# Kernel optimization log

Measured on AMD Instinct MI355X. Metric: run time of the kernel, lower is better.

## Reference

```python
import jax, jax.numpy as jnp
import numpy as np


def setup_inputs() -> dict:
    key = jax.random.key(0)
    ks = jax.random.split(key, 4)
    B, Tq, Tv, D = 8, 256, 512, 256  # decoder_dim = D = 256
    query = jax.random.normal(ks[0], (B, Tq, D), dtype=jnp.float32)
    value = jax.random.normal(ks[1], (B, Tv, D), dtype=jnp.float32)
    W1 = jax.random.normal(ks[2], (D, D), dtype=jnp.float32) * (1.0 / np.sqrt(D))
    b1 = jnp.zeros((D,), dtype=jnp.float32)
    W2 = jax.random.normal(ks[3], (D, D), dtype=jnp.float32) * (1.0 / np.sqrt(D))
    b2 = jnp.zeros((D,), dtype=jnp.float32)
    return {"query": query, "value": value, "W1": W1, "b1": b1, "W2": W2, "b2": b2}


def reference(query, value, W1, b1, W2, b2):
    # Dense projections: [B,Tq,D], [B,Tv,D]
    q = jnp.einsum('bqd,de->bqe', query, W1) + b1
    v = jnp.einsum('bvd,de->bve', value, W2) + b2
    # Additive (Bahdanau) score: broadcast tanh then reduce over feature dim
    # score: [B,Tq,Tv]  (intermediate [B,Tq,Tv,D] is the fusion target)
    score = jnp.tanh(q[:, :, None, :] + v[:, None, :, :]).sum(axis=-1)
    alignment = jax.nn.softmax(score, axis=-1)  # [B,Tq,Tv]
    context = jnp.einsum('bqv,bvd->bqd', alignment, value)  # [B,Tq,D]
    context = jnp.concatenate([context, query], axis=-1)  # [B,Tq,2D]
    alignment_t = jnp.transpose(alignment, (0, 2, 1))  # [B,Tv,Tq]
    return context, alignment_t
```

## Files before the change

kernel.cpp:

```cpp
#include <hip/hip_runtime.h>

#define B_  8
#define TQ  256
#define TV  512
#define DD  256
#define ALGS 520

__device__ __forceinline__ float fast_exp2(float x) {
#if __has_builtin(__builtin_amdgcn_exp2f)
  return __builtin_amdgcn_exp2f(x);
#else
  return __exp2f(x);
#endif
}
__device__ __forceinline__ float fast_rcp(float x) {
#if __has_builtin(__builtin_amdgcn_rcpf)
  return __builtin_amdgcn_rcpf(x);
#else
  return 1.0f / x;
#endif
}

__global__ __launch_bounds__(256) void proj_fused(
    const float* __restrict__ query, const float* __restrict__ value,
    const float* __restrict__ W1, const float* __restrict__ b1,
    const float* __restrict__ W2, const float* __restrict__ b2,
    float* __restrict__ qp, float* __restrict__ vp, float scale) {
  __shared__ float As[2][32][64];
  __shared__ float Bs[2][32][64];
  const int t  = threadIdx.x;
  const int rt = blockIdx.x;
  const int bn = blockIdx.y << 6;

  const float* A; const float* W; const float* bias; float* out; int row0;
  if (rt < 32) { row0 = rt << 6;        A = query; W = W1; bias = b1; out = qp; }
  else         { row0 = (rt - 32) << 6; A = value; W = W2; bias = b2; out = vp; }

  const int tx = t & 15, ty = t >> 4;
  const int aar = t >> 3, aac = (t & 7) << 2;
  const int bbr = t >> 4, bbc = (t & 15) << 2;

  float4 ra[2], rb[2];
#pragma unroll
  for (int it = 0; it < 2; ++it) {
    ra[it] = *(const float4*)(A + (size_t)(row0 + (it << 5) + aar) * DD + aac);
    rb[it] = *(const float4*)(W + (size_t)((it << 4) + bbr) * DD + bn + bbc);
  }
#pragma unroll
  for (int it = 0; it < 2; ++it) {
    const int m = (it << 5) + aar;
#pragma unroll
    for (int c = 0; c < 4; ++c) {
      const int k = aac + c;
      As[0][k][m ^ (((k >> 2) & 7) << 2)] = (&ra[it].x)[c];
    }
    *(float4*)&Bs[0][(it << 4) + bbr][bbc] = rb[it];
  }
  __syncthreads();

  float acc[4][4] = {{0.f,0.f,0.f,0.f},{0.f,0.f,0.f,0.f},
                     {0.f,0.f,0.f,0.f},{0.f,0.f,0.f,0.f}};
  int p = 0;

  for (int k0 = 0; k0 < 256; k0 += 32) {
    const bool more = (k0 + 32) < 256;
    if (more) {
#pragma unroll
      for (int it = 0; it < 2; ++it) {
        ra[it] = *(const float4*)(A + (size_t)(row0 + (it << 5) + aar) * DD + k0 + 32 + aac);
        rb[it] = *(const float4*)(W + (size_t)(k0 + 32 + (it << 4) + bbr) * DD + bn + bbc);
      }
    }
#pragma unroll
    for (int k = 0; k < 32; ++k) {
      float4 aq = *(const float4*)&As[p][k][(ty << 2) ^ (((k >> 2) & 7) << 2)];
      float4 bq = *(const float4*)&Bs[p][k][tx << 2];
      acc[0][0] = fmaf(aq.x, bq.x, acc[0][0]); acc[0][1] = fmaf(aq.x, bq.y, acc[0][1]);
      acc[0][2] = fmaf(aq.x, bq.z, acc[0][2]); acc[0][3] = fmaf(aq.x, bq.w, acc[0][3]);
      acc[1][0] = fmaf(aq.y, bq.x, acc[1][0]); acc[1][1] = fmaf(aq.y, bq.y, acc[1][1]);
      acc[1][2] = fmaf(aq.y, bq.z, acc[1][2]); acc[1][3] = fmaf(aq.y, bq.w, acc[1][3]);
      acc[2][0] = fmaf(aq.z, bq.x, acc[2][0]); acc[2][1] = fmaf(aq.z, bq.y, acc[2][1]);
      acc[2][2] = fmaf(aq.z, bq.z, acc[2][2]); acc[2][3] = fmaf(aq.z, bq.w, acc[2][3]);
      acc[3][0] = fmaf(aq.w, bq.x, acc[3][0]); acc[3][1] = fmaf(aq.w, bq.y, acc[3][1]);
      acc[3][2] = fmaf(aq.w, bq.z, acc[3][2]); acc[3][3] = fmaf(aq.w, bq.w, acc[3][3]);
    }
    if (more) {
      const int q = p ^ 1;
#pragma unroll
      for (int it = 0; it < 2; ++it) {
        const int m = (it << 5) + aar;
#pragma unroll
        for (int c = 0; c < 4; ++c) {
          const int k = aac + c;
          As[q][k][m ^ (((k >> 2) & 7) << 2)] = (&ra[it].x)[c];
        }
        *(float4*)&Bs[q][(it << 4) + bbr][bbc] = rb[it];
      }
      __syncthreads();
      p = q;
    }
  }

  float4 bvv = *(const float4*)&bias[bn + (tx << 2)];
#pragma unroll
  for (int r = 0; r < 4; ++r) {
    float4 o;
    o.x = fast_exp2(scale * (acc[r][0] + bvv.x));
    o.y = fast_exp2(scale * (acc[r][1] + bvv.y));
    o.z = fast_exp2(scale * (acc[r][2] + bvv.z));
    o.w = fast_exp2(scale * (acc[r][3] + bvv.w));
    *(float4*)(out + (size_t)(row0 + (ty << 2) + r) * DD + bn + (tx << 2)) = o;
  }
}

__global__ __launch_bounds__(512, 8) void attn_mono(
    const float* __restrict__ qp, const float* __restrict__ vp,
    const float* __restrict__ value, const float* __restrict__ query,
    float* __restrict__ out1, float* __restrict__ out2) {
  __shared__ float qs[4 * 256];
  __shared__ float alg[4 * ALGS];
  __shared__ float ctxp[8][4][128];

  const int t    = threadIdx.x;
  const int lane = t & 63;
  const int wv   = t >> 6;
  const int jj   = lane >> 2;
  const int dq   = lane & 3;
  const int bb   = blockIdx.x & 7;
  const int i0   = (blockIdx.x >> 3) << 2;

  const float* vpb = vp + (size_t)bb * TV * DD;
  const float* qb  = qp + (size_t)(bb * TQ + i0) * DD;

  {
    const int qi = t >> 7, qc = (t & 127) << 1;
    *(float2*)&qs[qi * 256 + qc] = *(const float2*)(qb + (size_t)qi * DD + qc);
  }
  __syncthreads();

  const int jb = (wv << 4) + jj;
  const float* vr0 = vpb + (size_t)jb * DD + (dq << 2);
  const float* vr1 = vr0 + 128 * DD;
  const float* vr2 = vr0 + 256 * DD;
  const float* vr3 = vr0 + 384 * DD;
  const float* qlane = qs + (dq << 2);

  float acc[4][4] = {{0.f,0.f,0.f,0.f},{0.f,0.f,0.f,0.f},
                     {0.f,0.f,0.f,0.f},{0.f,0.f,0.f,0.f}};

#pragma unroll 4
  for (int k = 0; k < 16; ++k) {
    const int doff = k << 4;
    float4 q0 = *(const float4*)(qlane + 0 * 256 + doff);
    float4 q1 = *(const float4*)(qlane + 1 * 256 + doff);
    float4 q2 = *(const float4*)(qlane + 2 * 256 + doff);
    float4 q3 = *(const float4*)(qlane + 3 * 256 + doff);
#pragma unroll
    for (int jg = 0; jg < 4; ++jg) {
      const float* vrp = (jg == 0) ? vr0 : (jg == 1) ? vr1 : (jg == 2) ? vr2 : vr3;
      float4 v4 = *(const float4*)(vrp + doff);
#pragma unroll
      for (int i = 0; i < 4; ++i) {
        const float4 q4 = (i == 0) ? q0 : (i == 1) ? q1 : (i == 2) ? q2 : q3;
        float a = q4.x * v4.x, b = q4.y * v4.y;
        float c = q4.z * v4.z, d = q4.w * v4.w;
        float sab = a + b,  scd = c + d;
        float Q1 = fmaf(a, b, sab + 1.f);
        float Q2 = fmaf(c, d, scd + 1.f);
        float N  = fmaf(scd + 2.f, Q1, (sab + 2.f) * Q2);
        acc[i][jg] = fmaf(N, fast_rcp(Q1 * Q2), acc[i][jg]);
      }
    }
  }

#pragma unroll
  for (int i = 0; i < 4; ++i)
#pragma unroll
    for (int jg = 0; jg < 4; ++jg) {
      acc[i][jg] += __shfl_xor(acc[i][jg], 1, 64);
      acc[i][jg] += __shfl_xor(acc[i][jg], 2, 64);
    }
#pragma unroll
  for (int jg = 0; jg < 4; ++jg) {
    float x = (dq == 0) ? acc[0][jg] : (dq == 1) ? acc[1][jg]
            : (dq == 2) ? acc[2][jg] : acc[3][jg];
    alg[dq * ALGS + (jg << 7) + jb] = x;
  }

  const int f4 = (t & 63) << 2;
  const int s  = t >> 6;
  const float* vb  = value + (size_t)bb * TV * DD;
  const float* vsp = vb + (size_t)(s << 6) * DD + f4;

  float4 pv0 = *(const float4*)(vsp + 0 * DD);
  float4 pv1 = *(const float4*)(vsp + 1 * DD);
  float4 pv2 = *(const float4*)(vsp + 2 * DD);
  float4 pv3 = *(const float4*)(vsp + 3 * DD);

  __syncthreads();

  if (wv < 4) {
    float sv[8];
#pragma unroll
    for (int c = 0; c < 8; ++c) sv[c] = alg[wv * ALGS + (c << 6) + lane];
    float mn = sv[0];
#pragma unroll
    for (int c = 1; c < 8; ++c) mn = fminf(mn, sv[c]);
#pragma unroll
    for (int m = 1; m < 64; m <<= 1) mn = fminf(mn, __shfl_xor(mn, m, 64));

    const float CC = 2.8853900817779268f;
    float p[8];
    float sum = 0.f;
#pragma unroll
    for (int c = 0; c < 8; ++c) { p[c] = fast_exp2(CC * (mn - sv[c])); sum += p[c]; }
#pragma unroll
    for (int m = 1; m < 64; m <<= 1) sum += __shfl_xor(sum, m, 64);
    const float inv = fast_rcp(sum);
#pragma unroll
    for (int c = 0; c < 8; ++c) alg[wv * ALGS + (c << 6) + lane] = p[c] * inv;
  }
  __syncthreads();

  {
    const int j = t;
    float4 av = make_float4(alg[j], alg[ALGS + j], alg[2 * ALGS + j], alg[3 * ALGS + j]);
    *(float4*)(out2 + (size_t)(bb * TV + j) * TQ + i0) = av;
  }

  float c4[4][4] = {{0.f,0.f,0.f,0.f},{0.f,0.f,0.f,0.f},
                    {0.f,0.f,0.f,0.f},{0.f,0.f,0.f,0.f}};
  const int jbase = s << 6;
  {
#pragma unroll
    for (int i = 0; i < 4; ++i) {
      float4 ai = *(const float4*)&alg[i * ALGS + jbase];
      c4[i][0] = fmaf(ai.x, pv0.x, c4[i][0]); c4[i][1] = fmaf(ai.x, pv0.y, c4[i][1]);
      c4[i][2] = fmaf(ai.x, pv0.z, c4[i][2]); c4[i][3] = fmaf(ai.x, pv0.w, c4[i][3]);
      c4[i][0] = fmaf(ai.y, pv1.x, c4[i][0]); c4[i][1] = fmaf(ai.y, pv1.y, c4[i][1]);
      c4[i][2] = fmaf(ai.y, pv1.z, c4[i][2]); c4[i][3] = fmaf(ai.y, pv1.w, c4[i][3]);
      c4[i][0] = fmaf(ai.z, pv2.x, c4[i][0]); c4[i][1] = fmaf(ai.z, pv2.y, c4[i][1]);
      c4[i][2] = fmaf(ai.z, pv2.z, c4[i][2]); c4[i][3] = fmaf(ai.z, pv2.w, c4[i][3]);
      c4[i][0] = fmaf(ai.w, pv3.x, c4[i][0]); c4[i][1] = fmaf(ai.w, pv3.y, c4[i][1]);
      c4[i][2] = fmaf(ai.w, pv3.z, c4[i][2]); c4[i][3] = fmaf(ai.w, pv3.w, c4[i][3]);
    }
  }
#pragma unroll 4
  for (int u = 4; u < 64; u += 4) {
    float4 v0 = *(const float4*)(vsp + (size_t)(u + 0) * DD);
    float4 v1 = *(const float4*)(vsp + (size_t)(u + 1) * DD);
    float4 v2 = *(const float4*)(vsp + (size_t)(u + 2) * DD);
    float4 v3 = *(const float4*)(vsp + (size_t)(u + 3) * DD);
#pragma unroll
    for (int i = 0; i < 4; ++i) {
      float4 ai = *(const float4*)&alg[i * ALGS + jbase + u];
      c4[i][0] = fmaf(ai.x, v0.x, c4[i][0]); c4[i][1] = fmaf(ai.x, v0.y, c4[i][1]);
      c4[i][2] = fmaf(ai.x, v0.z, c4[i][2]); c4[i][3] = fmaf(ai.x, v0.w, c4[i][3]);
      c4[i][0] = fmaf(ai.y, v1.x, c4[i][0]); c4[i][1] = fmaf(ai.y, v1.y, c4[i][1]);
      c4[i][2] = fmaf(ai.y, v1.z, c4[i][2]); c4[i][3] = fmaf(ai.y, v1.w, c4[i][3]);
      c4[i][0] = fmaf(ai.z, v2.x, c4[i][0]); c4[i][1] = fmaf(ai.z, v2.y, c4[i][1]);
      c4[i][2] = fmaf(ai.z, v2.z, c4[i][2]); c4[i][3] = fmaf(ai.z, v2.w, c4[i][3]);
      c4[i][0] = fmaf(ai.w, v3.x, c4[i][0]); c4[i][1] = fmaf(ai.w, v3.y, c4[i][1]);
      c4[i][2] = fmaf(ai.w, v3.z, c4[i][2]); c4[i][3] = fmaf(ai.w, v3.w, c4[i][3]);
    }
  }

  const float* qg = query + (size_t)(bb * TQ + i0) * DD;
  float* o = out1 + (size_t)(bb * TQ + i0) * (2 * DD);
#pragma unroll
  for (int h = 0; h < 2; ++h) {
    if ((f4 >> 7) == h) {
      const int fi = f4 & 127;
#pragma unroll
      for (int i = 0; i < 4; ++i)
        *(float4*)&ctxp[s][i][fi] = make_float4(c4[i][0], c4[i][1], c4[i][2], c4[i][3]);
    }
    __syncthreads();
    {
      const int ri = t >> 7;
      const int ff = t & 127;
      float sum = 0.f;
#pragma unroll
      for (int ss = 0; ss < 8; ++ss) sum += ctxp[ss][ri][ff];
      o[ri * 512 + (h << 7) + ff] = sum;
      o[ri * 512 + 256 + (h << 7) + ff] = qg[ri * DD + (h << 7) + ff];
    }
    if (h == 0) __syncthreads();
  }
}

extern "C" void kernel_launch(void* const* d_in, const int* in_sizes, int n_in,
                              void* d_out, int out_size, void* d_ws, size_t ws_size,
                              hipStream_t stream) {
  const float* query = (const float*)d_in[0];
  const float* value = (const float*)d_in[1];
  const float* W1    = (const float*)d_in[2];
  const float* b1    = (const float*)d_in[3];
  const float* W2    = (const float*)d_in[4];
  const float* b2    = (const float*)d_in[5];

  float* out1 = (float*)d_out;
  float* out2 = out1 + (size_t)B_ * TQ * 2 * DD;

  float* qp = (float*)d_ws;
  float* vp = qp + (size_t)B_ * TQ * DD;

  const float SC = 2.8853900817779268f;

  proj_fused<<<dim3(96, 4), 256, 0, stream>>>(query, value, W1, b1, W2, b2, qp, vp, SC);
  attn_mono<<<dim3(B_ * (TQ / 4)), 512, 0, stream>>>(qp, vp, value, query, out1, out2);
}
```

Measured before the change: 129.9 us.

## Double attention block to 1024 threads, splitting feature dimension across wave halves

The attention kernel now launches 1024 threads per block. The two halves of the block each compute the tanh score over half of the feature dimension and combine their partial scores in shared memory with an extra barrier. The context accumulation splits the value rows across 16 waves instead of 8. The goal is more parallelism per block, which shortens each thread's serial score loop. In exchange it adds a shared-memory add pass, another sync and a larger partial-context buffer, and at 1024 threads per block occupancy may be limited by registers.

```diff
diff --git a/kernel.cpp b/kernel.cpp
--- a/kernel.cpp
+++ b/kernel.cpp
@@ -113,17 +113,19 @@
   }
 }
 
-__global__ __launch_bounds__(512, 8) void attn_mono(
+__global__ __launch_bounds__(1024, 8) void attn_mono(
     const float* __restrict__ qp, const float* __restrict__ vp,
     const float* __restrict__ value, const float* __restrict__ query,
     float* __restrict__ out1, float* __restrict__ out2) {
   __shared__ float qs[4 * 256];
   __shared__ float alg[4 * ALGS];
-  __shared__ float ctxp[8][4][128];
+  __shared__ float ctxp[16][4][128];
 
   const int t    = threadIdx.x;
   const int lane = t & 63;
-  const int wv   = t >> 6;
+  const int w    = t >> 6;
+  const int wv   = w & 7;
+  const int dh   = w >> 3;
   const int jj   = lane >> 2;
   const int dq   = lane & 3;
   const int bb   = blockIdx.x & 7;
@@ -132,24 +134,22 @@
   const float* vpb = vp + (size_t)bb * TV * DD;
   const float* qb  = qp + (size_t)(bb * TQ + i0) * DD;
 
-  {
-    const int qi = t >> 7, qc = (t & 127) << 1;
-    *(float2*)&qs[qi * 256 + qc] = *(const float2*)(qb + (size_t)qi * DD + qc);
-  }
+  qs[t] = qb[(size_t)(t >> 8) * DD + (t & 255)];
   __syncthreads();
 
   const int jb = (wv << 4) + jj;
-  const float* vr0 = vpb + (size_t)jb * DD + (dq << 2);
+  const int d0 = dh << 7;
+  const float* vr0 = vpb + (size_t)jb * DD + d0 + (dq << 2);
   const float* vr1 = vr0 + 128 * DD;
   const float* vr2 = vr0 + 256 * DD;
   const float* vr3 = vr0 + 384 * DD;
-  const float* qlane = qs + (dq << 2);
+  const float* qlane = qs + d0 + (dq << 2);
 
   float acc[4][4] = {{0.f,0.f,0.f,0.f},{0.f,0.f,0.f,0.f},
                      {0.f,0.f,0.f,0.f},{0.f,0.f,0.f,0.f}};
 
 #pragma unroll 4
-  for (int k = 0; k < 16; ++k) {
+  for (int k = 0; k < 8; ++k) {
     const int doff = k << 4;
     float4 q0 = *(const float4*)(qlane + 0 * 256 + doff);
     float4 q1 = *(const float4*)(qlane + 1 * 256 + doff);
@@ -180,17 +180,22 @@
       acc[i][jg] += __shfl_xor(acc[i][jg], 1, 64);
       acc[i][jg] += __shfl_xor(acc[i][jg], 2, 64);
     }
-#pragma unroll
-  for (int jg = 0; jg < 4; ++jg) {
-    float x = (dq == 0) ? acc[0][jg] : (dq == 1) ? acc[1][jg]
-            : (dq == 2) ? acc[2][jg] : acc[3][jg];
-    alg[dq * ALGS + (jg << 7) + jb] = x;
+
+  float xh[4];
+#pragma unroll
+  for (int jg = 0; jg < 4; ++jg)
+    xh[jg] = (dq == 0) ? acc[0][jg] : (dq == 1) ? acc[1][jg]
+           : (dq == 2) ? acc[2][jg] : acc[3][jg];
+
+  if (dh == 0) {
+#pragma unroll
+    for (int jg = 0; jg < 4; ++jg) alg[dq * ALGS + (jg << 7) + jb] = xh[jg];
   }
 
   const int f4 = (t & 63) << 2;
   const int s  = t >> 6;
   const float* vb  = value + (size_t)bb * TV * DD;
-  const float* vsp = vb + (size_t)(s << 6) * DD + f4;
+  const float* vsp = vb + (size_t)(s << 5) * DD + f4;
 
   float4 pv0 = *(const float4*)(vsp + 0 * DD);
   float4 pv1 = *(const float4*)(vsp + 1 * DD);
@@ -198,11 +203,16 @@
   float4 pv3 = *(const float4*)(vsp + 3 * DD);
 
   __syncthreads();
-
-  if (wv < 4) {
+  if (dh == 1) {
+#pragma unroll
+    for (int jg = 0; jg < 4; ++jg) alg[dq * ALGS + (jg << 7) + jb] += xh[jg];
+  }
+  __syncthreads();
+
+  if (w < 4) {
     float sv[8];
 #pragma unroll
-    for (int c = 0; c < 8; ++c) sv[c] = alg[wv * ALGS + (c << 6) + lane];
+    for (int c = 0; c < 8; ++c) sv[c] = alg[w * ALGS + (c << 6) + lane];
     float mn = sv[0];
 #pragma unroll
     for (int c = 1; c < 8; ++c) mn = fminf(mn, sv[c]);
@@ -218,11 +228,11 @@
     for (int m = 1; m < 64; m <<= 1) sum += __shfl_xor(sum, m, 64);
     const float inv = fast_rcp(sum);
 #pragma unroll
-    for (int c = 0; c < 8; ++c) alg[wv * ALGS + (c << 6) + lane] = p[c] * inv;
-  }
-  __syncthreads();
-
-  {
+    for (int c = 0; c < 8; ++c) alg[w * ALGS + (c << 6) + lane] = p[c] * inv;
+  }
+  __syncthreads();
+
+  if (t < 512) {
     const int j = t;
     float4 av = make_float4(alg[j], alg[ALGS + j], alg[2 * ALGS + j], alg[3 * ALGS + j]);
     *(float4*)(out2 + (size_t)(bb * TV + j) * TQ + i0) = av;
@@ -230,7 +240,7 @@
 
   float c4[4][4] = {{0.f,0.f,0.f,0.f},{0.f,0.f,0.f,0.f},
                     {0.f,0.f,0.f,0.f},{0.f,0.f,0.f,0.f}};
-  const int jbase = s << 6;
+  const int jbase = s << 5;
   {
 #pragma unroll
     for (int i = 0; i < 4; ++i) {
@@ -245,8 +255,8 @@
       c4[i][2] = fmaf(ai.w, pv3.z, c4[i][2]); c4[i][3] = fmaf(ai.w, pv3.w, c4[i][3]);
     }
   }
-#pragma unroll 4
-  for (int u = 4; u < 64; u += 4) {
+#pragma unroll
+  for (int u = 4; u < 32; u += 4) {
     float4 v0 = *(const float4*)(vsp + (size_t)(u + 0) * DD);
     float4 v1 = *(const float4*)(vsp + (size_t)(u + 1) * DD);
     float4 v2 = *(const float4*)(vsp + (size_t)(u + 2) * DD);
@@ -276,12 +286,12 @@
         *(float4*)&ctxp[s][i][fi] = make_float4(c4[i][0], c4[i][1], c4[i][2], c4[i][3]);
     }
     __syncthreads();
-    {
+    if (t < 512) {
       const int ri = t >> 7;
       const int ff = t & 127;
       float sum = 0.f;
 #pragma unroll
-      for (int ss = 0; ss < 8; ++ss) sum += ctxp[ss][ri][ff];
+      for (int ss = 0; ss < 16; ++ss) sum += ctxp[ss][ri][ff];
       o[ri * 512 + (h << 7) + ff] = sum;
       o[ri * 512 + 256 + (h << 7) + ff] = qg[ri * DD + (h << 7) + ff];
     }
@@ -308,5 +318,5 @@
   const float SC = 2.8853900817779268f;
 
   proj_fused<<<dim3(96, 4), 256, 0, stream>>>(query, value, W1, b1, W2, b2, qp, vp, SC);
-  attn_mono<<<dim3(B_ * (TQ / 4)), 512, 0, stream>>>(qp, vp, value, query, out1, out2);
-}
+  attn_mono<<<dim3(B_ * (TQ / 4)), 1024, 0, stream>>>(qp, vp, value, query, out1, out2);
+}
```

Result: no change. 128.3 us (-1.3%).
